# Optimization experiments

Measured on AMD Instinct MI355X. Metric: run time of the kernel, lower is better.

Reference implementation:

```python
import jax, jax.numpy as jnp
import numpy as np

# Haar (db1) analysis filters, already time-reversed as in create_wavelet_filter
# (for Haar the synthesis filters coincide with the analysis filters).
_S = 0.5
DEC = jnp.array([[[ _S,  _S], [ _S,  _S]],   # LL
                 [[ _S,  _S], [-_S, -_S]],   # LH (lo along w, hi along h)
                 [[ _S, -_S], [ _S, -_S]],   # HL
                 [[ _S, -_S], [-_S,  _S]]],  # HH
                dtype=jnp.float32)


def dwconv3(x, w, b=None):
    """Depthwise 3x3 'same' conv. x: [B,C,H,W], w: [C,3,3]."""
    c = x.shape[1]
    y = jax.lax.conv_general_dilated(
        x, w[:, None], (1, 1), 'SAME',
        feature_group_count=c,
        dimension_numbers=('NCHW', 'OIHW', 'NCHW'))
    if b is not None:
        y = y + b[None, :, None, None]
    return y


def haar_dwt(x):
    """Stride-2 grouped Haar DWT. [B,C,H,W] -> [B,C,4,H/2,W/2]."""
    b, c, h, w = x.shape
    xr = x.reshape(b, c, h // 2, 2, w // 2, 2)
    return jnp.einsum('bcipjq,kpq->bckij', xr, DEC)


def haar_idwt(y):
    """Inverse Haar (conv_transpose stride 2, kernel 2 => non-overlapping)."""
    b, c, _, h2, w2 = y.shape
    out = jnp.einsum('bckij,kpq->bcipjq', y, DEC)
    return out.reshape(b, c, h2 * 2, w2 * 2)


def ln_cf(x, w, b, eps=1e-6):
    """ConvNeXt channels-first LayerNorm (mean/var over channel dim)."""
    u = jnp.mean(x, axis=1, keepdims=True)
    s = jnp.mean((x - u) ** 2, axis=1, keepdims=True)
    xn = (x - u) / jnp.sqrt(s + eps)
    return w[None, :, None, None] * xn + b[None, :, None, None]


def wtconv_dw(x, base_w, base_b, base_s, wt_w, wt_s):
    """WTConv2d depthwise path, wt_levels=1, db1. x: [B,C,H,W] (H,W even)."""
    b, c, h, w = x.shape
    cx = haar_dwt(x)                                  # [B,C,4,H/2,W/2]
    tag = cx.reshape(b, c * 4, h // 2, w // 2)
    tag = dwconv3(tag, wt_w) * wt_s[None, :, None, None]
    x_tag = haar_idwt(tag.reshape(b, c, 4, h // 2, w // 2))
    base = dwconv3(x, base_w, base_b) * base_s[None, :, None, None]
    return base + x_tag


def resize_mat(n_in, n_out):
    """Bilinear align_corners=True interpolation matrix [n_out, n_in]."""
    coords = jnp.arange(n_out, dtype=jnp.float32) * ((n_in - 1) / (n_out - 1))
    i0 = jnp.clip(jnp.floor(coords).astype(jnp.int32), 0, n_in - 2)
    f = coords - i0.astype(jnp.float32)
    r = jnp.arange(n_out)
    return (jnp.zeros((n_out, n_in), jnp.float32)
            .at[r, i0].add(1.0 - f)
            .at[r, i0 + 1].add(f))


def setup_inputs() -> dict:
    key = jax.random.key(0)
    ks = jax.random.split(key, 16)
    B, C_XH, C_XL = 8, 16, 8
    HH, HL = 256, 512
    g = C_XL // 2 + 1        # per-branch channels = 5
    ct = 2 * C_XL + 4        # tail channels = 20
    n = jax.random.normal
    return {
        'xh': n(ks[0], (B, C_XH, HH, HH), jnp.float32),
        'xl': n(ks[1], (B, C_XL, HL, HL), jnp.float32),
        'mask': jax.random.uniform(ks[2], (B, 1, HL, HL), jnp.float32),
        'pre_w': n(ks[3], (C_XL, C_XH), jnp.float32) * 0.25,
        'pre_b': n(ks[4], (C_XL,), jnp.float32) * 0.1,
        'g_ln_w': jnp.ones((4, g), jnp.float32),
        'g_ln_b': jnp.zeros((4, g), jnp.float32),
        'g_base_w': n(ks[5], (4, g, 3, 3), jnp.float32) * 0.3,
        'g_base_b': n(ks[6], (4, g), jnp.float32) * 0.1,
        'g_base_s': jnp.ones((4, g), jnp.float32),
        'g_wt_w': n(ks[7], (4, 4 * g, 3, 3), jnp.float32) * 0.3,
        'g_wt_s': jnp.full((4, 4 * g), 0.1, jnp.float32),
        'g_pw_w': n(ks[8], (4, g, g), jnp.float32) * 0.3,
        'tail_ln_w': jnp.ones((ct,), jnp.float32),
        'tail_ln_b': jnp.zeros((ct,), jnp.float32),
        'tail_w': n(ks[9], (C_XL, ct), jnp.float32) * 0.2,
        'tail_b': n(ks[10], (C_XL,), jnp.float32) * 0.1,
        'res_w': n(ks[11], (C_XL, C_XL + 1), jnp.float32) * 0.3,
        'res_b': n(ks[12], (C_XL,), jnp.float32) * 0.1,
    }


def reference(xh, xl, mask, pre_w, pre_b, g_ln_w, g_ln_b, g_base_w, g_base_b,
              g_base_s, g_wt_w, g_wt_s, g_pw_w, tail_ln_w, tail_ln_b,
              tail_w, tail_b, res_w, res_b):
    # pre_project: 1x1 conv dim_xh -> dim_xl (with bias)
    xh_p = jnp.einsum('oc,bchw->bohw', pre_w, xh) + pre_b[None, :, None, None]
    # bilinear upsample to xl spatial size, align_corners=True (separable)
    Mh = resize_mat(xh.shape[2], xl.shape[2])
    Mw = resize_mat(xh.shape[3], xl.shape[3])
    xh_u = jnp.einsum('Hh,bchw,Ww->bcHW', Mh, xh_p, Mw)
    # four branches: chunk xh/xl, concat with mask, LN_cf -> WTConv dw -> 1x1
    gs = xl.shape[1] // 4   # channels per chunk (2)
    outs = []
    for i in range(4):
        gi = jnp.concatenate(
            [xh_u[:, i * gs:(i + 1) * gs], xl[:, i * gs:(i + 1) * gs], mask],
            axis=1)                                   # [B, gs*2+1, H, W]
        gi = ln_cf(gi, g_ln_w[i], g_ln_b[i])
        gi = wtconv_dw(gi, g_base_w[i], g_base_b[i], g_base_s[i],
                       g_wt_w[i], g_wt_s[i])
        gi = jnp.einsum('oc,bchw->bohw', g_pw_w[i], gi)  # pointwise, no bias
        outs.append(gi)
    x = jnp.concatenate(outs, axis=1)                 # [B, 2*dim_xl+4, H, W]
    # tail: LN_cf -> 1x1 conv -> exact GELU
    x = ln_cf(x, tail_ln_w, tail_ln_b)
    x = jnp.einsum('oc,bchw->bohw', tail_w, x) + tail_b[None, :, None, None]
    x = jax.nn.gelu(x, approximate=False)
    # residual: 1x1 conv on cat(xl, mask)
    res = jnp.einsum('oc,bchw->bohw', res_w,
                     jnp.concatenate([xl, mask], axis=1))
    res = res + res_b[None, :, None, None]
    return x + res
```

## Files before the change

kernel.cpp:

```cpp
#include <hip/hip_runtime.h>
#include <math.h>

#define BB   8
#define CXH  16
#define CXL  8
#define HH   256
#define HL   512

#define TS   32
#define HALO 2
#define GT   (TS + 2*HALO)
#define GP   40

#define WS_PATCH_FLOATS (BB * 4 * HH * HH * 2)
#define WS_AB_OFF       WS_PATCH_FLOATS
#define WS_NEEDED_BYTES ((size_t)(WS_PATCH_FLOATS + 16) * sizeof(float))

__device__ __forceinline__ float gelu_fast(float x) {
    const float u = x * (1.595769122f + 0.071354816f * x * x);
    return x * __builtin_amdgcn_rcpf(1.0f + __expf(-u));
}

__global__ __launch_bounds__(256)
void pre_project_kernel(const float* __restrict__ xh,
                        const float* __restrict__ pre_w,
                        const float* __restrict__ pre_b,
                        const float* __restrict__ tail_ln_w,
                        const float* __restrict__ tail_ln_b,
                        const float* __restrict__ tail_w,
                        const float* __restrict__ tail_b,
                        float* __restrict__ ws)
{
    const int gid = blockIdx.x * 256 + threadIdx.x;
    const int b   = gid >> 16;
    const int px  = gid & 0xFFFF;
    const float* xp = xh + (b * CXH) * (HH * HH) + px;
    float xv[16];
    #pragma unroll
    for (int c = 0; c < 16; ++c) xv[c] = xp[c * HH * HH];
    #pragma unroll
    for (int br = 0; br < 4; ++br) {
        float a0 = pre_b[2 * br], a1 = pre_b[2 * br + 1];
        #pragma unroll
        for (int c = 0; c < 16; ++c) {
            a0 += pre_w[(2 * br) * 16 + c] * xv[c];
            a1 += pre_w[(2 * br + 1) * 16 + c] * xv[c];
        }
        float2 r; r.x = a0; r.y = a1;
        *(float2*)&ws[((b * 4 + br) * (HH * HH) + px) * 2] = r;
    }
    if (gid < 8) {
        const int o = gid;
        float a = 0.f, bb = tail_b[o];
        for (int cg = 0; cg < 20; ++cg) {
            a  += tail_w[o * 20 + cg] * tail_ln_w[cg];
            bb += tail_w[o * 20 + cg] * tail_ln_b[cg];
        }
        ws[WS_AB_OFF + o]     = a;
        ws[WS_AB_OFF + 8 + o] = bb;
    }
}

template <bool USE_WS>
__global__ __launch_bounds__(256, 3)
void uem_fused_kernel(const float* __restrict__ xh,
                      const float* __restrict__ xl,
                      const float* __restrict__ mask,
                      const float* __restrict__ pre_w,
                      const float* __restrict__ pre_b,
                      const float* __restrict__ g_ln_w,
                      const float* __restrict__ g_ln_b,
                      const float* __restrict__ g_base_w,
                      const float* __restrict__ g_base_b,
                      const float* __restrict__ g_base_s,
                      const float* __restrict__ g_wt_w,
                      const float* __restrict__ g_wt_s,
                      const float* __restrict__ g_pw_w,
                      const float* __restrict__ tail_ln_w,
                      const float* __restrict__ tail_ln_b,
                      const float* __restrict__ tail_w,
                      const float* __restrict__ tail_b,
                      const float* __restrict__ res_w,
                      const float* __restrict__ res_b,
                      const float* __restrict__ ws,
                      float* __restrict__ out)
{
    __shared__ __align__(16) float s_gln[5][GT][GP];

    const int b   = blockIdx.z;
    const int ty0 = blockIdx.y * TS;
    const int tx0 = blockIdx.x * TS;
    const int tx  = threadIdx.x, ty = threadIdx.y;
    const int tid = ty * 16 + tx;

    const float SC = (float)(255.0 / 511.0);

    float S1[4] = {0.f, 0.f, 0.f, 0.f};
    float S2[4] = {0.f, 0.f, 0.f, 0.f};
    float T[4][8];
    #pragma unroll
    for (int p = 0; p < 4; ++p)
        #pragma unroll
        for (int o = 0; o < 8; ++o) T[p][o] = 0.f;

    for (int br = 0; br < 4; ++br) {
        for (int idx = tid; idx < GT * GT; idx += 256) {
            const int ly = idx / GT, lx = idx % GT;
            const int gy = ty0 - HALO + ly, gx = tx0 - HALO + lx;
            float vv[5] = {0.f, 0.f, 0.f, 0.f, 0.f};
            if (gy >= 0 && gy < HL && gx >= 0 && gx < HL) {
                const float cy = (float)gy * SC;
                const int iy0 = min((int)cy, HH - 2);
                const float fy = cy - (float)iy0;
                const float cx = (float)gx * SC;
                const int ix0 = min((int)cx, HH - 2);
                const float fx = cx - (float)ix0;
                float2 q00, q01, q10, q11;
                if (USE_WS) {
                    const float* wsp = ws + ((size_t)(b * 4 + br) * (HH * HH)) * 2;
                    q00 = *(const float2*)&wsp[(iy0 * HH + ix0) * 2];
                    q01 = *(const float2*)&wsp[(iy0 * HH + ix0 + 1) * 2];
                    q10 = *(const float2*)&wsp[((iy0 + 1) * HH + ix0) * 2];
                    q11 = *(const float2*)&wsp[((iy0 + 1) * HH + ix0 + 1) * 2];
                } else {
                    #pragma unroll
                    for (int q = 0; q < 4; ++q) {
                        const int iy = iy0 + (q >> 1), ix = ix0 + (q & 1);
                        const float* xp = xh + ((b * CXH) * HH + iy) * HH + ix;
                        float a0 = pre_b[2 * br], a1 = pre_b[2 * br + 1];
                        #pragma unroll
                        for (int c = 0; c < 16; ++c) {
                            const float v = xp[c * HH * HH];
                            a0 += pre_w[(2 * br) * 16 + c] * v;
                            a1 += pre_w[(2 * br + 1) * 16 + c] * v;
                        }
                        float2 r; r.x = a0; r.y = a1;
                        if (q == 0) q00 = r; else if (q == 1) q01 = r;
                        else if (q == 2) q10 = r; else q11 = r;
                    }
                }
                {
                    const float top = q00.x + fx * (q01.x - q00.x);
                    const float bot = q10.x + fx * (q11.x - q10.x);
                    vv[0] = top + fy * (bot - top);
                }
                {
                    const float top = q00.y + fx * (q01.y - q00.y);
                    const float bot = q10.y + fx * (q11.y - q10.y);
                    vv[1] = top + fy * (bot - top);
                }
                const int xbase = ((b * CXL) * HL + gy) * HL + gx;
                vv[2] = xl[xbase + (2 * br) * HL * HL];
                vv[3] = xl[xbase + (2 * br + 1) * HL * HL];
                vv[4] = mask[(b * HL + gy) * HL + gx];
                const float u = (vv[0] + vv[1] + vv[2] + vv[3] + vv[4]) * 0.2f;
                float var = 0.f;
                #pragma unroll
                for (int c = 0; c < 5; ++c) { const float d = vv[c] - u; var += d * d; }
                var *= 0.2f;
                const float rstd = rsqrtf(var + 1e-6f);
                #pragma unroll
                for (int c = 0; c < 5; ++c)
                    vv[c] = g_ln_w[br * 5 + c] * ((vv[c] - u) * rstd) + g_ln_b[br * 5 + c];
            }
            #pragma unroll
            for (int c = 0; c < 5; ++c) s_gln[c][ly][lx] = vv[c];
        }
        __syncthreads();

        const float* wb = g_wt_w + br * 180;
        float gi[5][4];
        #pragma unroll
        for (int c = 0; c < 5; ++c) {
            float P[6][6];
            #pragma unroll
            for (int r = 0; r < 6; ++r) {
                const float* rp = &s_gln[c][2 * ty + r][2 * tx];
                const float2 pa = *(const float2*)(rp);
                const float2 pb = *(const float2*)(rp + 2);
                const float2 pc = *(const float2*)(rp + 4);
                P[r][0] = pa.x; P[r][1] = pa.y;
                P[r][2] = pb.x; P[r][3] = pb.y;
                P[r][4] = pc.x; P[r][5] = pc.y;
            }
            float tc0 = 0.f, tc1 = 0.f, tc2 = 0.f, tc3 = 0.f;
            #pragma unroll
            for (int dy = 0; dy < 3; ++dy) {
                #pragma unroll
                for (int dx = 0; dx < 3; ++dx) {
                    const float a  = P[2 * dy][2 * dx];
                    const float b2 = P[2 * dy][2 * dx + 1];
                    const float c2 = P[2 * dy + 1][2 * dx];
                    const float d2 = P[2 * dy + 1][2 * dx + 1];
                    const float s0 = a + b2, s1 = c2 + d2;
                    const float d0 = a - b2, d1 = c2 - d2;
                    const int wo = dy * 3 + dx;
                    tc0 += wb[(c * 4 + 0) * 9 + wo] * (s0 + s1);
                    tc1 += wb[(c * 4 + 1) * 9 + wo] * (s0 - s1);
                    tc2 += wb[(c * 4 + 2) * 9 + wo] * (d0 + d1);
                    tc3 += wb[(c * 4 + 3) * 9 + wo] * (d0 - d1);
                }
            }
            const float t0 = tc0 * (0.5f * g_wt_s[br * 20 + c * 4 + 0]);
            const float t1 = tc1 * (0.5f * g_wt_s[br * 20 + c * 4 + 1]);
            const float t2 = tc2 * (0.5f * g_wt_s[br * 20 + c * 4 + 2]);
            const float t3 = tc3 * (0.5f * g_wt_s[br * 20 + c * 4 + 3]);
            const float xt0 = 0.5f * (t0 + t1 + t2 + t3);
            const float xt1 = 0.5f * (t0 + t1 - t2 - t3);
            const float xt2 = 0.5f * (t0 - t1 + t2 - t3);
            const float xt3 = 0.5f * (t0 - t1 - t2 + t3);
            const float* bw = g_base_w + br * 45 + c * 9;
            const float bb2 = g_base_b[br * 5 + c], bs = g_base_s[br * 5 + c];
            #pragma unroll
            for (int p = 0; p < 4; ++p) {
                const int py = p >> 1, px = p & 1;
                float acc = 0.f;
                #pragma unroll
                for (int dy = 0; dy < 3; ++dy)
                    #pragma unroll
                    for (int dx = 0; dx < 3; ++dx)
                        acc += bw[dy * 3 + dx] * P[1 + py + dy][1 + px + dx];
                const float xtv = (p == 0) ? xt0 : (p == 1) ? xt1 : (p == 2) ? xt2 : xt3;
                gi[c][p] = (acc + bb2) * bs + xtv;
            }
        }

        #pragma unroll
        for (int o = 0; o < 5; ++o) {
            const int cg = br * 5 + o;
            float v[4];
            #pragma unroll
            for (int p = 0; p < 4; ++p) {
                float vv = 0.f;
                #pragma unroll
                for (int c = 0; c < 5; ++c) vv += g_pw_w[br * 25 + o * 5 + c] * gi[c][p];
                v[p] = vv;
                S1[p] += vv;
                S2[p] += vv * vv;
            }
            const float lw = tail_ln_w[cg];
            #pragma unroll
            for (int o8 = 0; o8 < 8; ++o8) {
                const float w = tail_w[o8 * 20 + cg] * lw;
                T[0][o8] += w * v[0];
                T[1][o8] += w * v[1];
                T[2][o8] += w * v[2];
                T[3][o8] += w * v[3];
            }
        }
        __syncthreads();
    }

    float A[8], Bc[8];
    if (USE_WS) {
        #pragma unroll
        for (int o = 0; o < 8; ++o) {
            A[o]  = ws[WS_AB_OFF + o];
            Bc[o] = ws[WS_AB_OFF + 8 + o];
        }
    } else {
        #pragma unroll
        for (int o = 0; o < 8; ++o) {
            float a = 0.f, bb = tail_b[o];
            #pragma unroll
            for (int cg = 0; cg < 20; ++cg) {
                a  += tail_w[o * 20 + cg] * tail_ln_w[cg];
                bb += tail_w[o * 20 + cg] * tail_ln_b[cg];
            }
            A[o] = a; Bc[o] = bb;
        }
    }

    #pragma unroll
    for (int py = 0; py < 2; ++py) {
        const int p0 = py * 2, p1 = py * 2 + 1;
        const int gy  = ty0 + 2 * ty + py;
        const int gx0 = tx0 + 2 * tx;
        const float u0    = S1[p0] * 0.05f;
        const float u1    = S1[p1] * 0.05f;
        const float rstd0 = rsqrtf(S2[p0] * 0.05f - u0 * u0 + 1e-6f);
        const float rstd1 = rsqrtf(S2[p1] * 0.05f - u1 * u1 + 1e-6f);

        const int xbase = ((b * CXL) * HL + gy) * HL + gx0;
        float2 xlv[8];
        #pragma unroll
        for (int c = 0; c < 8; ++c) xlv[c] = *(const float2*)&xl[xbase + c * HL * HL];
        const float2 mk = *(const float2*)&mask[(b * HL + gy) * HL + gx0];

        #pragma unroll
        for (int o = 0; o < 8; ++o) {
            const float val0 = (T[p0][o] - u0 * A[o]) * rstd0 + Bc[o];
            const float val1 = (T[p1][o] - u1 * A[o]) * rstd1 + Bc[o];
            float r0 = res_b[o] + res_w[o * 9 + 8] * mk.x;
            float r1 = res_b[o] + res_w[o * 9 + 8] * mk.y;
            #pragma unroll
            for (int c = 0; c < 8; ++c) {
                r0 += res_w[o * 9 + c] * xlv[c].x;
                r1 += res_w[o * 9 + c] * xlv[c].y;
            }
            float2 ov;
            ov.x = gelu_fast(val0) + r0;
            ov.y = gelu_fast(val1) + r1;
            *(float2*)&out[xbase + o * HL * HL] = ov;
        }
    }
}

extern "C" void kernel_launch(void* const* d_in, const int* in_sizes, int n_in,
                              void* d_out, int out_size, void* d_ws, size_t ws_size,
                              hipStream_t stream) {
    (void)in_sizes; (void)out_size;
    if (n_in < 19) return;
    const float* xh        = (const float*)d_in[0];
    const float* xl        = (const float*)d_in[1];
    const float* mask      = (const float*)d_in[2];
    const float* pre_w     = (const float*)d_in[3];
    const float* pre_b     = (const float*)d_in[4];
    const float* g_ln_w    = (const float*)d_in[5];
    const float* g_ln_b    = (const float*)d_in[6];
    const float* g_base_w  = (const float*)d_in[7];
    const float* g_base_b  = (const float*)d_in[8];
    const float* g_base_s  = (const float*)d_in[9];
    const float* g_wt_w    = (const float*)d_in[10];
    const float* g_wt_s    = (const float*)d_in[11];
    const float* g_pw_w    = (const float*)d_in[12];
    const float* tail_ln_w = (const float*)d_in[13];
    const float* tail_ln_b = (const float*)d_in[14];
    const float* tail_w    = (const float*)d_in[15];
    const float* tail_b    = (const float*)d_in[16];
    const float* res_w     = (const float*)d_in[17];
    const float* res_b     = (const float*)d_in[18];
    float* outp = (float*)d_out;
    float* ws   = (float*)d_ws;

    dim3 grid(HL / TS, HL / TS, BB);
    dim3 block(16, 16, 1);

    const bool use_ws = (ws != nullptr) && (ws_size >= WS_NEEDED_BYTES);
    if (use_ws) {
        pre_project_kernel<<<dim3(2048), dim3(256), 0, stream>>>(
            xh, pre_w, pre_b, tail_ln_w, tail_ln_b, tail_w, tail_b, ws);
        uem_fused_kernel<true><<<grid, block, 0, stream>>>(
            xh, xl, mask, pre_w, pre_b, g_ln_w, g_ln_b, g_base_w, g_base_b,
            g_base_s, g_wt_w, g_wt_s, g_pw_w, tail_ln_w, tail_ln_b, tail_w,
            tail_b, res_w, res_b, ws, outp);
    } else {
        uem_fused_kernel<false><<<grid, block, 0, stream>>>(
            xh, xl, mask, pre_w, pre_b, g_ln_w, g_ln_b, g_base_w, g_base_b,
            g_base_s, g_wt_w, g_wt_s, g_pw_w, tail_ln_w, tail_ln_b, tail_w,
            tail_b, res_w, res_b, ws, outp);
    }
}
```

Before: 319.1 us.

## Split fused kernel into per-branch kernel and per-pixel tail kernel via workspace

When the workspace is large enough, the single fused kernel is replaced by two kernels. A branch kernel runs one block per (batch, branch, tile) and writes the 20 branch outputs to a large workspace buffer. A tail kernel then does the tail LayerNorm, 1x1 conv, GELU and residual per pixel. This aims to raise parallelism and cut per-thread register pressure, at the cost of a large round trip through global memory for the intermediate.

New measurement: 481.5 us. +50.9%, slower.

```diff
diff --git a/kernel.cpp b/kernel.cpp
--- a/kernel.cpp
+++ b/kernel.cpp
@@ -14,7 +14,10 @@
 
 #define WS_PATCH_FLOATS (BB * 4 * HH * HH * 2)
 #define WS_AB_OFF       WS_PATCH_FLOATS
-#define WS_NEEDED_BYTES ((size_t)(WS_PATCH_FLOATS + 16) * sizeof(float))
+#define WS_VB_OFF       (WS_AB_OFF + 16)
+#define WS_VB_FLOATS    ((size_t)BB * 20 * HL * HL)
+#define WS_SMALL_BYTES  ((size_t)(WS_PATCH_FLOATS + 16) * sizeof(float))
+#define WS_BIG_BYTES    (((size_t)WS_PATCH_FLOATS + 16 + WS_VB_FLOATS) * sizeof(float))
 
 __device__ __forceinline__ float gelu_fast(float x) {
     const float u = x * (1.595769122f + 0.071354816f * x * x);
@@ -58,6 +61,207 @@
         }
         ws[WS_AB_OFF + o]     = a;
         ws[WS_AB_OFF + 8 + o] = bb;
+    }
+}
+
+__global__ __launch_bounds__(256, 3)
+void branch_kernel(const float* __restrict__ xl,
+                   const float* __restrict__ mask,
+                   const float* __restrict__ g_ln_w,
+                   const float* __restrict__ g_ln_b,
+                   const float* __restrict__ g_base_w,
+                   const float* __restrict__ g_base_b,
+                   const float* __restrict__ g_base_s,
+                   const float* __restrict__ g_wt_w,
+                   const float* __restrict__ g_wt_s,
+                   const float* __restrict__ g_pw_w,
+                   float* __restrict__ ws)
+{
+    __shared__ __align__(16) float s_gln[5][GT][GP];
+
+    const int bz  = blockIdx.z;
+    const int b   = bz >> 2;
+    const int br  = bz & 3;
+    const int ty0 = blockIdx.y * TS;
+    const int tx0 = blockIdx.x * TS;
+    const int tx  = threadIdx.x, ty = threadIdx.y;
+    const int tid = ty * 16 + tx;
+
+    const float SC = (float)(255.0 / 511.0);
+
+    const float* wsp = ws + ((size_t)(b * 4 + br) * (HH * HH)) * 2;
+    for (int idx = tid; idx < GT * GT; idx += 256) {
+        const int ly = idx / GT, lx = idx % GT;
+        const int gy = ty0 - HALO + ly, gx = tx0 - HALO + lx;
+        float vv[5] = {0.f, 0.f, 0.f, 0.f, 0.f};
+        if (gy >= 0 && gy < HL && gx >= 0 && gx < HL) {
+            const float cy = (float)gy * SC;
+            const int iy0 = min((int)cy, HH - 2);
+            const float fy = cy - (float)iy0;
+            const float cx = (float)gx * SC;
+            const int ix0 = min((int)cx, HH - 2);
+            const float fx = cx - (float)ix0;
+            const float2 q00 = *(const float2*)&wsp[(iy0 * HH + ix0) * 2];
+            const float2 q01 = *(const float2*)&wsp[(iy0 * HH + ix0 + 1) * 2];
+            const float2 q10 = *(const float2*)&wsp[((iy0 + 1) * HH + ix0) * 2];
+            const float2 q11 = *(const float2*)&wsp[((iy0 + 1) * HH + ix0 + 1) * 2];
+            {
+                const float top = q00.x + fx * (q01.x - q00.x);
+                const float bot = q10.x + fx * (q11.x - q10.x);
+                vv[0] = top + fy * (bot - top);
+            }
+            {
+                const float top = q00.y + fx * (q01.y - q00.y);
+                const float bot = q10.y + fx * (q11.y - q10.y);
+                vv[1] = top + fy * (bot - top);
+            }
+            const int xbase = ((b * CXL) * HL + gy) * HL + gx;
+            vv[2] = xl[xbase + (2 * br) * HL * HL];
+            vv[3] = xl[xbase + (2 * br + 1) * HL * HL];
+            vv[4] = mask[(b * HL + gy) * HL + gx];
+            const float u = (vv[0] + vv[1] + vv[2] + vv[3] + vv[4]) * 0.2f;
+            float var = 0.f;
+            #pragma unroll
+            for (int c = 0; c < 5; ++c) { const float d = vv[c] - u; var += d * d; }
+            var *= 0.2f;
+            const float rstd = rsqrtf(var + 1e-6f);
+            #pragma unroll
+            for (int c = 0; c < 5; ++c)
+                vv[c] = g_ln_w[br * 5 + c] * ((vv[c] - u) * rstd) + g_ln_b[br * 5 + c];
+        }
+        #pragma unroll
+        for (int c = 0; c < 5; ++c) s_gln[c][ly][lx] = vv[c];
+    }
+    __syncthreads();
+
+    const float* wb = g_wt_w + br * 180;
+    float gi[5][4];
+    #pragma unroll
+    for (int c = 0; c < 5; ++c) {
+        float P[6][6];
+        #pragma unroll
+        for (int r = 0; r < 6; ++r) {
+            const float* rp = &s_gln[c][2 * ty + r][2 * tx];
+            const float2 pa = *(const float2*)(rp);
+            const float2 pb = *(const float2*)(rp + 2);
+            const float2 pc = *(const float2*)(rp + 4);
+            P[r][0] = pa.x; P[r][1] = pa.y;
+            P[r][2] = pb.x; P[r][3] = pb.y;
+            P[r][4] = pc.x; P[r][5] = pc.y;
+        }
+        float tc0 = 0.f, tc1 = 0.f, tc2 = 0.f, tc3 = 0.f;
+        #pragma unroll
+        for (int dy = 0; dy < 3; ++dy) {
+            #pragma unroll
+            for (int dx = 0; dx < 3; ++dx) {
+                const float a  = P[2 * dy][2 * dx];
+                const float b2 = P[2 * dy][2 * dx + 1];
+                const float c2 = P[2 * dy + 1][2 * dx];
+                const float d2 = P[2 * dy + 1][2 * dx + 1];
+                const float s0 = a + b2, s1 = c2 + d2;
+                const float d0 = a - b2, d1 = c2 - d2;
+                const int wo = dy * 3 + dx;
+                tc0 += wb[(c * 4 + 0) * 9 + wo] * (s0 + s1);
+                tc1 += wb[(c * 4 + 1) * 9 + wo] * (s0 - s1);
+                tc2 += wb[(c * 4 + 2) * 9 + wo] * (d0 + d1);
+                tc3 += wb[(c * 4 + 3) * 9 + wo] * (d0 - d1);
+            }
+        }
+        const float t0 = tc0 * (0.5f * g_wt_s[br * 20 + c * 4 + 0]);
+        const float t1 = tc1 * (0.5f * g_wt_s[br * 20 + c * 4 + 1]);
+        const float t2 = tc2 * (0.5f * g_wt_s[br * 20 + c * 4 + 2]);
+        const float t3 = tc3 * (0.5f * g_wt_s[br * 20 + c * 4 + 3]);
+        const float xt0 = 0.5f * (t0 + t1 + t2 + t3);
+        const float xt1 = 0.5f * (t0 + t1 - t2 - t3);
+        const float xt2 = 0.5f * (t0 - t1 + t2 - t3);
+        const float xt3 = 0.5f * (t0 - t1 - t2 + t3);
+        const float* bw = g_base_w + br * 45 + c * 9;
+        const float bb2 = g_base_b[br * 5 + c], bs = g_base_s[br * 5 + c];
+        #pragma unroll
+        for (int p = 0; p < 4; ++p) {
+            const int py = p >> 1, px = p & 1;
+            float acc = 0.f;
+            #pragma unroll
+            for (int dy = 0; dy < 3; ++dy)
+                #pragma unroll
+                for (int dx = 0; dx < 3; ++dx)
+                    acc += bw[dy * 3 + dx] * P[1 + py + dy][1 + px + dx];
+            const float xtv = (p == 0) ? xt0 : (p == 1) ? xt1 : (p == 2) ? xt2 : xt3;
+            gi[c][p] = (acc + bb2) * bs + xtv;
+        }
+    }
+
+    const size_t vplane = (size_t)HL * HL;
+    float* vb = ws + WS_VB_OFF + (size_t)(b * 20 + br * 5) * vplane;
+    const int gy0 = ty0 + 2 * ty;
+    const int gx0 = tx0 + 2 * tx;
+    #pragma unroll
+    for (int o = 0; o < 5; ++o) {
+        float v[4];
+        #pragma unroll
+        for (int p = 0; p < 4; ++p) {
+            float vv = 0.f;
+            #pragma unroll
+            for (int c = 0; c < 5; ++c) vv += g_pw_w[br * 25 + o * 5 + c] * gi[c][p];
+            v[p] = vv;
+        }
+        float* op = vb + o * vplane + gy0 * HL + gx0;
+        float2 r0; r0.x = v[0]; r0.y = v[1];
+        float2 r1; r1.x = v[2]; r1.y = v[3];
+        *(float2*)(op)      = r0;
+        *(float2*)(op + HL) = r1;
+    }
+}
+
+__global__ __launch_bounds__(256)
+void tail_kernel(const float* __restrict__ xl,
+                 const float* __restrict__ mask,
+                 const float* __restrict__ tail_ln_w,
+                 const float* __restrict__ tail_w,
+                 const float* __restrict__ res_w,
+                 const float* __restrict__ res_b,
+                 const float* __restrict__ ws,
+                 float* __restrict__ out)
+{
+    const int gid = blockIdx.x * 256 + threadIdx.x;
+    const int b   = gid >> 18;
+    const int pix = gid & 0x3FFFF;
+    const size_t vplane = (size_t)HL * HL;
+
+    const float* vb = ws + WS_VB_OFF + (size_t)b * 20 * vplane + pix;
+    float vw[20];
+    float s = 0.f;
+    #pragma unroll
+    for (int cg = 0; cg < 20; ++cg) {
+        const float v = vb[cg * vplane];
+        vw[cg] = v;
+        s += v;
+    }
+    const float u = s * 0.05f;
+    float var = 0.f;
+    #pragma unroll
+    for (int cg = 0; cg < 20; ++cg) { const float d = vw[cg] - u; var += d * d; }
+    const float rstd = rsqrtf(var * 0.05f + 1e-6f);
+    #pragma unroll
+    for (int cg = 0; cg < 20; ++cg) vw[cg] *= tail_ln_w[cg];
+
+    const float* xp = xl + (size_t)(b * CXL) * vplane + pix;
+    float xlv[8];
+    #pragma unroll
+    for (int c = 0; c < 8; ++c) xlv[c] = xp[c * vplane];
+    const float mk = mask[(size_t)b * vplane + pix];
+
+    float* op = out + (size_t)(b * CXL) * vplane + pix;
+    #pragma unroll
+    for (int o = 0; o < 8; ++o) {
+        float t = 0.f;
+        #pragma unroll
+        for (int cg = 0; cg < 20; ++cg) t += tail_w[o * 20 + cg] * vw[cg];
+        const float val = (t - u * ws[WS_AB_OFF + o]) * rstd + ws[WS_AB_OFF + 8 + o];
+        float r = res_b[o] + res_w[o * 9 + 8] * mk;
+        #pragma unroll
+        for (int c = 0; c < 8; ++c) r += res_w[o * 9 + c] * xlv[c];
+        op[o * vplane] = gelu_fast(val) + r;
     }
 }
 
@@ -333,19 +537,25 @@
     float* outp = (float*)d_out;
     float* ws   = (float*)d_ws;
 
-    dim3 grid(HL / TS, HL / TS, BB);
     dim3 block(16, 16, 1);
 
-    const bool use_ws = (ws != nullptr) && (ws_size >= WS_NEEDED_BYTES);
-    if (use_ws) {
+    if (ws != nullptr && ws_size >= WS_BIG_BYTES) {
         pre_project_kernel<<<dim3(2048), dim3(256), 0, stream>>>(
             xh, pre_w, pre_b, tail_ln_w, tail_ln_b, tail_w, tail_b, ws);
-        uem_fused_kernel<true><<<grid, block, 0, stream>>>(
+        branch_kernel<<<dim3(HL / TS, HL / TS, BB * 4), block, 0, stream>>>(
+            xl, mask, g_ln_w, g_ln_b, g_base_w, g_base_b, g_base_s,
+            g_wt_w, g_wt_s, g_pw_w, ws);
+        tail_kernel<<<dim3(BB * HL * HL / 256), dim3(256), 0, stream>>>(
+            xl, mask, tail_ln_w, tail_w, res_w, res_b, ws, outp);
+    } else if (ws != nullptr && ws_size >= WS_SMALL_BYTES) {
+        pre_project_kernel<<<dim3(2048), dim3(256), 0, stream>>>(
+            xh, pre_w, pre_b, tail_ln_w, tail_ln_b, tail_w, tail_b, ws);
+        uem_fused_kernel<true><<<dim3(HL / TS, HL / TS, BB), block, 0, stream>>>(
             xh, xl, mask, pre_w, pre_b, g_ln_w, g_ln_b, g_base_w, g_base_b,
             g_base_s, g_wt_w, g_wt_s, g_pw_w, tail_ln_w, tail_ln_b, tail_w,
             tail_b, res_w, res_b, ws, outp);
     } else {
-        uem_fused_kernel<false><<<grid, block, 0, stream>>>(
+        uem_fused_kernel<false><<<dim3(HL / TS, HL / TS, BB), block, 0, stream>>>(
             xh, xl, mask, pre_w, pre_b, g_ln_w, g_ln_b, g_base_w, g_base_b,
             g_base_s, g_wt_w, g_wt_s, g_pw_w, tail_ln_w, tail_ln_b, tail_w,
             tail_b, res_w, res_b, ws, outp);
```

## Process branches in pairs with quad-interleaved shared layout and fewer barriers

Applied to the files above, without the earlier changes.

The fused kernel now stages two branches per tile-load pass. It shares the mask load, the bilinear coordinates and the loop index math between the two branches, and it needs only one barrier between pairs instead of two per branch. Shared memory is stored as 2x2 quads so each thread reads its patch with float4 loads instead of strided float2 loads. The fallback path without a workspace is removed, so the kernel now returns without output when the workspace is missing, and doubling the shared footprint may reduce occupancy.

New measurement: 296.6 us. 1.08x faster.

```diff
diff --git a/kernel.cpp b/kernel.cpp
--- a/kernel.cpp
+++ b/kernel.cpp
@@ -10,7 +10,7 @@
 #define TS   32
 #define HALO 2
 #define GT   (TS + 2*HALO)
-#define GP   40
+#define NPX  (GT * GT)
 
 #define WS_PATCH_FLOATS (BB * 4 * HH * HH * 2)
 #define WS_AB_OFF       WS_PATCH_FLOATS
@@ -19,6 +19,17 @@
 __device__ __forceinline__ float gelu_fast(float x) {
     const float u = x * (1.595769122f + 0.071354816f * x * x);
     return x * __builtin_amdgcn_rcpf(1.0f + __expf(-u));
+}
+
+__device__ __forceinline__ void ln5(float* vv, const float* w, const float* bta) {
+    const float u = (vv[0] + vv[1] + vv[2] + vv[3] + vv[4]) * 0.2f;
+    float var = 0.f;
+    #pragma unroll
+    for (int c = 0; c < 5; ++c) { const float d = vv[c] - u; var += d * d; }
+    var *= 0.2f;
+    const float rstd = rsqrtf(var + 1e-6f);
+    #pragma unroll
+    for (int c = 0; c < 5; ++c) vv[c] = w[c] * ((vv[c] - u) * rstd) + bta[c];
 }
 
 __global__ __launch_bounds__(256)
@@ -61,31 +72,25 @@
     }
 }
 
-template <bool USE_WS>
 __global__ __launch_bounds__(256, 3)
-void uem_fused_kernel(const float* __restrict__ xh,
-                      const float* __restrict__ xl,
-                      const float* __restrict__ mask,
-                      const float* __restrict__ pre_w,
-                      const float* __restrict__ pre_b,
-                      const float* __restrict__ g_ln_w,
-                      const float* __restrict__ g_ln_b,
-                      const float* __restrict__ g_base_w,
-                      const float* __restrict__ g_base_b,
-                      const float* __restrict__ g_base_s,
-                      const float* __restrict__ g_wt_w,
-                      const float* __restrict__ g_wt_s,
-                      const float* __restrict__ g_pw_w,
-                      const float* __restrict__ tail_ln_w,
-                      const float* __restrict__ tail_ln_b,
-                      const float* __restrict__ tail_w,
-                      const float* __restrict__ tail_b,
-                      const float* __restrict__ res_w,
-                      const float* __restrict__ res_b,
-                      const float* __restrict__ ws,
-                      float* __restrict__ out)
+void uem_pair_kernel(const float* __restrict__ xl,
+                     const float* __restrict__ mask,
+                     const float* __restrict__ g_ln_w,
+                     const float* __restrict__ g_ln_b,
+                     const float* __restrict__ g_base_w,
+                     const float* __restrict__ g_base_b,
+                     const float* __restrict__ g_base_s,
+                     const float* __restrict__ g_wt_w,
+                     const float* __restrict__ g_wt_s,
+                     const float* __restrict__ g_pw_w,
+                     const float* __restrict__ tail_ln_w,
+                     const float* __restrict__ tail_w,
+                     const float* __restrict__ res_w,
+                     const float* __restrict__ res_b,
+                     const float* __restrict__ ws,
+                     float* __restrict__ out)
 {
-    __shared__ __align__(16) float s_gln[5][GT][GP];
+    __shared__ __align__(16) float s_q[2][5][18][18][4];
 
     const int b   = blockIdx.z;
     const int ty0 = blockIdx.y * TS;
@@ -94,6 +99,9 @@
     const int tid = ty * 16 + tx;
 
     const float SC = (float)(255.0 / 511.0);
+    const int plane = HL * HL;
+    const int mb  = b * plane;
+    const int xlb = (b * CXL) * plane;
 
     float S1[4] = {0.f, 0.f, 0.f, 0.f};
     float S2[4] = {0.f, 0.f, 0.f, 0.f};
@@ -103,11 +111,14 @@
         #pragma unroll
         for (int o = 0; o < 8; ++o) T[p][o] = 0.f;
 
-    for (int br = 0; br < 4; ++br) {
-        for (int idx = tid; idx < GT * GT; idx += 256) {
-            const int ly = idx / GT, lx = idx % GT;
+    for (int pair = 0; pair < 2; ++pair) {
+        const float* wsp0 = ws + ((size_t)(b * 4 + 2 * pair)     * (HH * HH)) * 2;
+        const float* wsp1 = ws + ((size_t)(b * 4 + 2 * pair + 1) * (HH * HH)) * 2;
+        int ly = tid / 36, lx = tid % 36;
+        for (int idx = tid; idx < NPX; idx += 256) {
             const int gy = ty0 - HALO + ly, gx = tx0 - HALO + lx;
-            float vv[5] = {0.f, 0.f, 0.f, 0.f, 0.f};
+            float va[5] = {0.f, 0.f, 0.f, 0.f, 0.f};
+            float vb[5] = {0.f, 0.f, 0.f, 0.f, 0.f};
             if (gy >= 0 && gy < HL && gx >= 0 && gx < HL) {
                 const float cy = (float)gy * SC;
                 const int iy0 = min((int)cy, HH - 2);
@@ -115,160 +126,151 @@
                 const float cx = (float)gx * SC;
                 const int ix0 = min((int)cx, HH - 2);
                 const float fx = cx - (float)ix0;
-                float2 q00, q01, q10, q11;
-                if (USE_WS) {
-                    const float* wsp = ws + ((size_t)(b * 4 + br) * (HH * HH)) * 2;
-                    q00 = *(const float2*)&wsp[(iy0 * HH + ix0) * 2];
-                    q01 = *(const float2*)&wsp[(iy0 * HH + ix0 + 1) * 2];
-                    q10 = *(const float2*)&wsp[((iy0 + 1) * HH + ix0) * 2];
-                    q11 = *(const float2*)&wsp[((iy0 + 1) * HH + ix0 + 1) * 2];
-                } else {
+                const int co  = (iy0 * HH + ix0) * 2;
+                const int pix = gy * HL + gx;
+                const float mk = mask[mb + pix];
+                {
+                    const float2 q00 = *(const float2*)&wsp0[co];
+                    const float2 q01 = *(const float2*)&wsp0[co + 2];
+                    const float2 q10 = *(const float2*)&wsp0[co + 2 * HH];
+                    const float2 q11 = *(const float2*)&wsp0[co + 2 * HH + 2];
+                    {
+                        const float top = q00.x + fx * (q01.x - q00.x);
+                        const float bot = q10.x + fx * (q11.x - q10.x);
+                        va[0] = top + fy * (bot - top);
+                    }
+                    {
+                        const float top = q00.y + fx * (q01.y - q00.y);
+                        const float bot = q10.y + fx * (q11.y - q10.y);
+                        va[1] = top + fy * (bot - top);
+                    }
+                    va[2] = xl[xlb + (4 * pair + 0) * plane + pix];
+                    va[3] = xl[xlb + (4 * pair + 1) * plane + pix];
+                    va[4] = mk;
+                    ln5(va, g_ln_w + (2 * pair) * 5, g_ln_b + (2 * pair) * 5);
+                }
+                {
+                    const float2 q00 = *(const float2*)&wsp1[co];
+                    const float2 q01 = *(const float2*)&wsp1[co + 2];
+                    const float2 q10 = *(const float2*)&wsp1[co + 2 * HH];
+                    const float2 q11 = *(const float2*)&wsp1[co + 2 * HH + 2];
+                    {
+                        const float top = q00.x + fx * (q01.x - q00.x);
+                        const float bot = q10.x + fx * (q11.x - q10.x);
+                        vb[0] = top + fy * (bot - top);
+                    }
+                    {
+                        const float top = q00.y + fx * (q01.y - q00.y);
+                        const float bot = q10.y + fx * (q11.y - q10.y);
+                        vb[1] = top + fy * (bot - top);
+                    }
+                    vb[2] = xl[xlb + (4 * pair + 2) * plane + pix];
+                    vb[3] = xl[xlb + (4 * pair + 3) * plane + pix];
+                    vb[4] = mk;
+                    ln5(vb, g_ln_w + (2 * pair + 1) * 5, g_ln_b + (2 * pair + 1) * 5);
+                }
+            }
+            const int qy = ly >> 1, qx = lx >> 1, sub = (ly & 1) * 2 + (lx & 1);
+            #pragma unroll
+            for (int c = 0; c < 5; ++c) s_q[0][c][qy][qx][sub] = va[c];
+            #pragma unroll
+            for (int c = 0; c < 5; ++c) s_q[1][c][qy][qx][sub] = vb[c];
+            lx += 4; ly += 7;
+            if (lx >= 36) { lx -= 36; ly += 1; }
+        }
+        __syncthreads();
+
+        for (int s = 0; s < 2; ++s) {
+            const int br = 2 * pair + s;
+            const float* wb = g_wt_w + br * 180;
+            float gi[5][4];
+            #pragma unroll
+            for (int c = 0; c < 5; ++c) {
+                float P[6][6];
+                #pragma unroll
+                for (int a = 0; a < 3; ++a)
                     #pragma unroll
-                    for (int q = 0; q < 4; ++q) {
-                        const int iy = iy0 + (q >> 1), ix = ix0 + (q & 1);
-                        const float* xp = xh + ((b * CXH) * HH + iy) * HH + ix;
-                        float a0 = pre_b[2 * br], a1 = pre_b[2 * br + 1];
+                    for (int bq = 0; bq < 3; ++bq) {
+                        const float4 q = *(const float4*)&s_q[s][c][ty + a][tx + bq][0];
+                        P[2 * a][2 * bq]         = q.x;
+                        P[2 * a][2 * bq + 1]     = q.y;
+                        P[2 * a + 1][2 * bq]     = q.z;
+                        P[2 * a + 1][2 * bq + 1] = q.w;
+                    }
+                float tc0 = 0.f, tc1 = 0.f, tc2 = 0.f, tc3 = 0.f;
+                #pragma unroll
+                for (int dy = 0; dy < 3; ++dy) {
+                    #pragma unroll
+                    for (int dx = 0; dx < 3; ++dx) {
+                        const float a  = P[2 * dy][2 * dx];
+                        const float b2 = P[2 * dy][2 * dx + 1];
+                        const float c2 = P[2 * dy + 1][2 * dx];
+                        const float d2 = P[2 * dy + 1][2 * dx + 1];
+                        const float s0 = a + b2, s1 = c2 + d2;
+                        const float d0 = a - b2, d1 = c2 - d2;
+                        const int wo = dy * 3 + dx;
+                        tc0 += wb[(c * 4 + 0) * 9 + wo] * (s0 + s1);
+                        tc1 += wb[(c * 4 + 1) * 9 + wo] * (s0 - s1);
+                        tc2 += wb[(c * 4 + 2) * 9 + wo] * (d0 + d1);
+                        tc3 += wb[(c * 4 + 3) * 9 + wo] * (d0 - d1);
+                    }
+                }
+                const float t0 = tc0 * (0.5f * g_wt_s[br * 20 + c * 4 + 0]);
+                const float t1 = tc1 * (0.5f * g_wt_s[br * 20 + c * 4 + 1]);
+                const float t2 = tc2 * (0.5f * g_wt_s[br * 20 + c * 4 + 2]);
+                const float t3 = tc3 * (0.5f * g_wt_s[br * 20 + c * 4 + 3]);
+                const float xt0 = 0.5f * (t0 + t1 + t2 + t3);
+                const float xt1 = 0.5f * (t0 + t1 - t2 - t3);
+                const float xt2 = 0.5f * (t0 - t1 + t2 - t3);
+                const float xt3 = 0.5f * (t0 - t1 - t2 + t3);
+                const float* bw = g_base_w + br * 45 + c * 9;
+                const float bb2 = g_base_b[br * 5 + c], bs = g_base_s[br * 5 + c];
+                #pragma unroll
+                for (int p = 0; p < 4; ++p) {
+                    const int py = p >> 1, px = p & 1;
+                    float acc = 0.f;
+                    #pragma unroll
+                    for (int dy = 0; dy < 3; ++dy)
                         #pragma unroll
-                        for (int c = 0; c < 16; ++c) {
-                            const float v = xp[c * HH * HH];
-                            a0 += pre_w[(2 * br) * 16 + c] * v;
-                            a1 += pre_w[(2 * br + 1) * 16 + c] * v;
-                        }
-                        float2 r; r.x = a0; r.y = a1;
-                        if (q == 0) q00 = r; else if (q == 1) q01 = r;
-                        else if (q == 2) q10 = r; else q11 = r;
-                    }
-                }
-                {
-                    const float top = q00.x + fx * (q01.x - q00.x);
-                    const float bot = q10.x + fx * (q11.x - q10.x);
-                    vv[0] = top + fy * (bot - top);
-                }
-                {
-                    const float top = q00.y + fx * (q01.y - q00.y);
-                    const float bot = q10.y + fx * (q11.y - q10.y);
-                    vv[1] = top + fy * (bot - top);
-                }
-                const int xbase = ((b * CXL) * HL + gy) * HL + gx;
-                vv[2] = xl[xbase + (2 * br) * HL * HL];
-                vv[3] = xl[xbase + (2 * br + 1) * HL * HL];
-                vv[4] = mask[(b * HL + gy) * HL + gx];
-                const float u = (vv[0] + vv[1] + vv[2] + vv[3] + vv[4]) * 0.2f;
-                float var = 0.f;
-                #pragma unroll
-                for (int c = 0; c < 5; ++c) { const float d = vv[c] - u; var += d * d; }
-                var *= 0.2f;
-                const float rstd = rsqrtf(var + 1e-6f);
-                #pragma unroll
-                for (int c = 0; c < 5; ++c)
-                    vv[c] = g_ln_w[br * 5 + c] * ((vv[c] - u) * rstd) + g_ln_b[br * 5 + c];
+                        for (int dx = 0; dx < 3; ++dx)
+                            acc += bw[dy * 3 + dx] * P[1 + py + dy][1 + px + dx];
+                    const float xtv = (p == 0) ? xt0 : (p == 1) ? xt1 : (p == 2) ? xt2 : xt3;
+                    gi[c][p] = (acc + bb2) * bs + xtv;
+                }
             }
-            #pragma unroll
-            for (int c = 0; c < 5; ++c) s_gln[c][ly][lx] = vv[c];
-        }
-        __syncthreads();
-
-        const float* wb = g_wt_w + br * 180;
-        float gi[5][4];
-        #pragma unroll
-        for (int c = 0; c < 5; ++c) {
-            float P[6][6];
-            #pragma unroll
-            for (int r = 0; r < 6; ++r) {
-                const float* rp = &s_gln[c][2 * ty + r][2 * tx];
-                const float2 pa = *(const float2*)(rp);
-                const float2 pb = *(const float2*)(rp + 2);
-                const float2 pc = *(const float2*)(rp + 4);
-                P[r][0] = pa.x; P[r][1] = pa.y;
-                P[r][2] = pb.x; P[r][3] = pb.y;
-                P[r][4] = pc.x; P[r][5] = pc.y;
+
+            #pragma unroll
+            for (int o = 0; o < 5; ++o) {
+                const int cg = br * 5 + o;
+                float v[4];
+                #pragma unroll
+                for (int p = 0; p < 4; ++p) {
+                    float vv = 0.f;
+                    #pragma unroll
+                    for (int c = 0; c < 5; ++c) vv += g_pw_w[br * 25 + o * 5 + c] * gi[c][p];
+                    v[p] = vv;
+                    S1[p] += vv;
+                    S2[p] += vv * vv;
+                }
+                const float lw = tail_ln_w[cg];
+                #pragma unroll
+                for (int o8 = 0; o8 < 8; ++o8) {
+                    const float w = tail_w[o8 * 20 + cg] * lw;
+                    T[0][o8] += w * v[0];
+                    T[1][o8] += w * v[1];
+                    T[2][o8] += w * v[2];
+                    T[3][o8] += w * v[3];
+                }
             }
-            float tc0 = 0.f, tc1 = 0.f, tc2 = 0.f, tc3 = 0.f;
-            #pragma unroll
-            for (int dy = 0; dy < 3; ++dy) {
-                #pragma unroll
-                for (int dx = 0; dx < 3; ++dx) {
-                    const float a  = P[2 * dy][2 * dx];
-                    const float b2 = P[2 * dy][2 * dx + 1];
-                    const float c2 = P[2 * dy + 1][2 * dx];
-                    const float d2 = P[2 * dy + 1][2 * dx + 1];
-                    const float s0 = a + b2, s1 = c2 + d2;
-                    const float d0 = a - b2, d1 = c2 - d2;
-                    const int wo = dy * 3 + dx;
-                    tc0 += wb[(c * 4 + 0) * 9 + wo] * (s0 + s1);
-                    tc1 += wb[(c * 4 + 1) * 9 + wo] * (s0 - s1);
-                    tc2 += wb[(c * 4 + 2) * 9 + wo] * (d0 + d1);
-                    tc3 += wb[(c * 4 + 3) * 9 + wo] * (d0 - d1);
-                }
-            }
-            const float t0 = tc0 * (0.5f * g_wt_s[br * 20 + c * 4 + 0]);
-            const float t1 = tc1 * (0.5f * g_wt_s[br * 20 + c * 4 + 1]);
-            const float t2 = tc2 * (0.5f * g_wt_s[br * 20 + c * 4 + 2]);
-            const float t3 = tc3 * (0.5f * g_wt_s[br * 20 + c * 4 + 3]);
-            const float xt0 = 0.5f * (t0 + t1 + t2 + t3);
-            const float xt1 = 0.5f * (t0 + t1 - t2 - t3);
-            const float xt2 = 0.5f * (t0 - t1 + t2 - t3);
-            const float xt3 = 0.5f * (t0 - t1 - t2 + t3);
-            const float* bw = g_base_w + br * 45 + c * 9;
-            const float bb2 = g_base_b[br * 5 + c], bs = g_base_s[br * 5 + c];
-            #pragma unroll
-            for (int p = 0; p < 4; ++p) {
-                const int py = p >> 1, px = p & 1;
-                float acc = 0.f;
-                #pragma unroll
-                for (int dy = 0; dy < 3; ++dy)
-                    #pragma unroll
-                    for (int dx = 0; dx < 3; ++dx)
-                        acc += bw[dy * 3 + dx] * P[1 + py + dy][1 + px + dx];
-                const float xtv = (p == 0) ? xt0 : (p == 1) ? xt1 : (p == 2) ? xt2 : xt3;
-                gi[c][p] = (acc + bb2) * bs + xtv;
-            }
-        }
-
-        #pragma unroll
-        for (int o = 0; o < 5; ++o) {
-            const int cg = br * 5 + o;
-            float v[4];
-            #pragma unroll
-            for (int p = 0; p < 4; ++p) {
-                float vv = 0.f;
-                #pragma unroll
-                for (int c = 0; c < 5; ++c) vv += g_pw_w[br * 25 + o * 5 + c] * gi[c][p];
-                v[p] = vv;
-                S1[p] += vv;
-                S2[p] += vv * vv;
-            }
-            const float lw = tail_ln_w[cg];
-            #pragma unroll
-            for (int o8 = 0; o8 < 8; ++o8) {
-                const float w = tail_w[o8 * 20 + cg] * lw;
-                T[0][o8] += w * v[0];
-                T[1][o8] += w * v[1];
-                T[2][o8] += w * v[2];
-                T[3][o8] += w * v[3];
-            }
-        }
-        __syncthreads();
+        }
+        if (pair == 0) __syncthreads();
     }
 
     float A[8], Bc[8];
-    if (USE_WS) {
-        #pragma unroll
-        for (int o = 0; o < 8; ++o) {
-            A[o]  = ws[WS_AB_OFF + o];
-            Bc[o] = ws[WS_AB_OFF + 8 + o];
-        }
-    } else {
-        #pragma unroll
-        for (int o = 0; o < 8; ++o) {
-            float a = 0.f, bb = tail_b[o];
-            #pragma unroll
-            for (int cg = 0; cg < 20; ++cg) {
-                a  += tail_w[o * 20 + cg] * tail_ln_w[cg];
-                bb += tail_w[o * 20 + cg] * tail_ln_b[cg];
-            }
-            A[o] = a; Bc[o] = bb;
-        }
+    #pragma unroll
+    for (int o = 0; o < 8; ++o) {
+        A[o]  = ws[WS_AB_OFF + o];
+        Bc[o] = ws[WS_AB_OFF + 8 + o];
     }
 
     #pragma unroll
@@ -281,11 +283,11 @@
         const float rstd0 = rsqrtf(S2[p0] * 0.05f - u0 * u0 + 1e-6f);
         const float rstd1 = rsqrtf(S2[p1] * 0.05f - u1 * u1 + 1e-6f);
 
-        const int xbase = ((b * CXL) * HL + gy) * HL + gx0;
+        const int xbase = xlb + gy * HL + gx0;
         float2 xlv[8];
         #pragma unroll
-        for (int c = 0; c < 8; ++c) xlv[c] = *(const float2*)&xl[xbase + c * HL * HL];
-        const float2 mk = *(const float2*)&mask[(b * HL + gy) * HL + gx0];
+        for (int c = 0; c < 8; ++c) xlv[c] = *(const float2*)&xl[xbase + c * plane];
+        const float2 mk = *(const float2*)&mask[mb + gy * HL + gx0];
 
         #pragma unroll
         for (int o = 0; o < 8; ++o) {
@@ -301,7 +303,7 @@
             float2 ov;
             ov.x = gelu_fast(val0) + r0;
             ov.y = gelu_fast(val1) + r1;
-            *(float2*)&out[xbase + o * HL * HL] = ov;
+            *(float2*)&out[xbase + o * plane] = ov;
         }
     }
 }
@@ -333,21 +335,11 @@
     float* outp = (float*)d_out;
     float* ws   = (float*)d_ws;
 
-    dim3 grid(HL / TS, HL / TS, BB);
-    dim3 block(16, 16, 1);
-
-    const bool use_ws = (ws != nullptr) && (ws_size >= WS_NEEDED_BYTES);
-    if (use_ws) {
-        pre_project_kernel<<<dim3(2048), dim3(256), 0, stream>>>(
-            xh, pre_w, pre_b, tail_ln_w, tail_ln_b, tail_w, tail_b, ws);
-        uem_fused_kernel<true><<<grid, block, 0, stream>>>(
-            xh, xl, mask, pre_w, pre_b, g_ln_w, g_ln_b, g_base_w, g_base_b,
-            g_base_s, g_wt_w, g_wt_s, g_pw_w, tail_ln_w, tail_ln_b, tail_w,
-            tail_b, res_w, res_b, ws, outp);
-    } else {
-        uem_fused_kernel<false><<<grid, block, 0, stream>>>(
-            xh, xl, mask, pre_w, pre_b, g_ln_w, g_ln_b, g_base_w, g_base_b,
-            g_base_s, g_wt_w, g_wt_s, g_pw_w, tail_ln_w, tail_ln_b, tail_w,
-            tail_b, res_w, res_b, ws, outp);
-    }
-}
+    if (ws == nullptr || ws_size < WS_NEEDED_BYTES) return;
+
+    pre_project_kernel<<<dim3(2048), dim3(256), 0, stream>>>(
+        xh, pre_w, pre_b, tail_ln_w, tail_ln_b, tail_w, tail_b, ws);
+    uem_pair_kernel<<<dim3(HL / TS, HL / TS, BB), dim3(16, 16, 1), 0, stream>>>(
+        xl, mask, g_ln_w, g_ln_b, g_base_w, g_base_b, g_base_s,
+        g_wt_w, g_wt_s, g_pw_w, tail_ln_w, tail_w, res_w, res_b, ws, outp);
+}
```
